# Kernel optimization log

Measured on AMD Instinct MI355X. Metric: run time of the kernel, lower is better.

Reference implementation:

```python
import jax, jax.numpy as jnp
import numpy as np

B, N, C = 4, 1029, 1024
H = 16           # num_heads
L = 8            # num_blocks
DH = C // H      # head_dim = 64
HID = 4 * C      # mlp hidden
SCALE = DH ** -0.5
EPS = 1e-6


def _ln(x, w, b):
    mu = jnp.mean(x, axis=-1, keepdims=True)
    var = jnp.var(x, axis=-1, keepdims=True)
    return (x - mu) * jax.lax.rsqrt(var + EPS) * w + b


def setup_inputs() -> dict:
    key = jax.random.key(0)
    ks = jax.random.split(key, 16)
    s = 0.02
    return {
        "x": jax.random.normal(ks[0], (B, N, C), dtype=jnp.float32),
        "ln1_w": jnp.ones((L, C), jnp.float32),
        "ln1_b": jnp.zeros((L, C), jnp.float32),
        "qkv_w": jax.random.normal(ks[1], (L, 3 * C, C), jnp.float32) * s,
        "qkv_b": jnp.zeros((L, 3 * C), jnp.float32),
        "proj_w": jax.random.normal(ks[2], (L, C, C), jnp.float32) * s,
        "proj_b": jnp.zeros((L, C), jnp.float32),
        "ln2_w": jnp.ones((L, C), jnp.float32),
        "ln2_b": jnp.zeros((L, C), jnp.float32),
        "fc1_w": jax.random.normal(ks[3], (L, HID, C), jnp.float32) * s,
        "fc1_b": jnp.zeros((L, HID), jnp.float32),
        "fc2_w": jax.random.normal(ks[4], (L, C, HID), jnp.float32) * s,
        "fc2_b": jnp.zeros((L, C), jnp.float32),
        "norm_w": jnp.ones((C,), jnp.float32),
        "norm_b": jnp.zeros((C,), jnp.float32),
    }


def _block(x, p):
    ln1_w, ln1_b, qkv_w, qkv_b, proj_w, proj_b, ln2_w, ln2_b, fc1_w, fc1_b, fc2_w, fc2_b = p
    # --- attention (manual fp32 QK^T / softmax / AV, as in Attention.forward) ---
    h = _ln(x, ln1_w, ln1_b)
    qkv = h @ qkv_w.T + qkv_b                        # [B,N,3C]
    qkv = qkv.reshape(B, N, 3, H, DH).transpose(2, 0, 3, 1, 4)  # [3,B,H,N,DH]
    q, k, v = qkv[0], qkv[1], qkv[2]
    attn = jnp.einsum("bhnd,bhmd->bhnm", q.astype(jnp.float32), k.astype(jnp.float32)) * SCALE
    # original subtracts row max before softmax; jax.nn.softmax is the same stable math
    attn = jax.nn.softmax(attn, axis=-1).astype(v.dtype)
    o = jnp.einsum("bhnm,bhmd->bhnd", attn, v)       # [B,H,N,DH]
    o = o.transpose(0, 2, 1, 3).reshape(B, N, C)
    x = x + (o @ proj_w.T + proj_b)
    # --- MLP (exact GELU, as nn.GELU default) ---
    h = _ln(x, ln2_w, ln2_b)
    h = jax.nn.gelu(h @ fc1_w.T + fc1_b, approximate=False)
    x = x + (h @ fc2_w.T + fc2_b)
    return x


def reference(x, ln1_w, ln1_b, qkv_w, qkv_b, proj_w, proj_b, ln2_w, ln2_b,
              fc1_w, fc1_b, fc2_w, fc2_b, norm_w, norm_b):
    params = (ln1_w, ln1_b, qkv_w, qkv_b, proj_w, proj_b, ln2_w, ln2_b,
              fc1_w, fc1_b, fc2_w, fc2_b)

    def body(h, p):
        return _block(h, p), None

    x, _ = jax.lax.scan(body, x, params)
    return _ln(x, norm_w, norm_b)
```

## Files before the change

kernel.cpp:

```cpp
#include <hip/hip_runtime.h>
#include <cstdint>
#include <cstddef>

#define B_    4
#define N_TOK 1029
#define C_    1024
#define H_    16
#define L_    8
#define HID_  4096
#define M_TOK (B_*N_TOK)
#define MP2_  4352
#define TM0_  4096
#define PROWS 4224
#define KVB_  128
#define KVT2_ 9
#define KPAD_ 1152

typedef float f32x4 __attribute__((ext_vector_type(4)));
typedef short bf16x8 __attribute__((ext_vector_type(8)));

__device__ __forceinline__ uint16_t f2bf(float f) {
  uint32_t u = __float_as_uint(f);
  u += 0x7fffu + ((u >> 16) & 1u);
  return (uint16_t)(u >> 16);
}

__device__ __forceinline__ void async_copy16(const uint16_t* src, uint16_t* lds_dst) {
  __builtin_amdgcn_global_load_lds(
      (const __attribute__((address_space(1))) void*)src,
      (__attribute__((address_space(3))) void*)lds_dst, 16, 0, 0);
}

__device__ __forceinline__ int swz16(int row, int byte_in_row) {
  return row * 128 + (byte_in_row ^ ((row & 7) << 4));
}

__global__ __launch_bounds__(256)
void cvt_f32_bf16(const float* __restrict__ in, uint16_t* __restrict__ out, int n4) {
  int i = blockIdx.x * 256 + threadIdx.x;
  if (i < n4) {
    float4 v = reinterpret_cast<const float4*>(in)[i];
    uint64_t pk = (uint64_t)f2bf(v.x) | ((uint64_t)f2bf(v.y) << 16)
                | ((uint64_t)f2bf(v.z) << 32) | ((uint64_t)f2bf(v.w) << 48);
    reinterpret_cast<uint64_t*>(out)[i] = pk;
  }
}

template<int OUTMODE>
__global__ __launch_bounds__(256)
void ln_fwd(const float* __restrict__ x, const float* __restrict__ w,
            const float* __restrict__ b, void* __restrict__ outp) {
  const int row = blockIdx.x;
  const int tid = threadIdx.x;
  const float4 v = reinterpret_cast<const float4*>(x + (size_t)row * C_)[tid];
  float s  = v.x + v.y + v.z + v.w;
  float s2 = v.x*v.x + v.y*v.y + v.z*v.z + v.w*v.w;
  #pragma unroll
  for (int d = 1; d < 64; d <<= 1) {
    s  += __shfl_xor(s, d);
    s2 += __shfl_xor(s2, d);
  }
  __shared__ float red[8];
  const int wv = tid >> 6;
  if ((tid & 63) == 0) { red[wv] = s; red[wv + 4] = s2; }
  __syncthreads();
  s  = red[0] + red[1] + red[2] + red[3];
  s2 = red[4] + red[5] + red[6] + red[7];
  const float mu = s * (1.0f / C_);
  const float rs = rsqrtf(fmaxf(s2 * (1.0f / C_) - mu * mu, 0.0f) + 1e-6f);
  const float4 wv4 = reinterpret_cast<const float4*>(w)[tid];
  const float4 bv4 = reinterpret_cast<const float4*>(b)[tid];
  const float o0 = (v.x - mu) * rs * wv4.x + bv4.x;
  const float o1 = (v.y - mu) * rs * wv4.y + bv4.y;
  const float o2 = (v.z - mu) * rs * wv4.z + bv4.z;
  const float o3 = (v.w - mu) * rs * wv4.w + bv4.w;
  uint64_t pk = (uint64_t)f2bf(o0) | ((uint64_t)f2bf(o1) << 16)
              | ((uint64_t)f2bf(o2) << 32) | ((uint64_t)f2bf(o3) << 48);
  reinterpret_cast<uint64_t*>((uint16_t*)outp + (size_t)row * C_)[tid] = pk;
}

template<int KCH, int OUT>
__global__ __launch_bounds__(256)
void reduce_ln(const float* __restrict__ pbuf, const float* __restrict__ bias,
               float* __restrict__ xbuf, const float* __restrict__ lw,
               const float* __restrict__ lb, void* __restrict__ outp) {
  const int m = blockIdx.x;
  const int c4 = threadIdx.x;
  float4 s = reinterpret_cast<const float4*>(bias)[c4];
  #pragma unroll
  for (int kc = 0; kc < KCH; ++kc) {
    const float4 pv = reinterpret_cast<const float4*>(pbuf + ((size_t)kc * PROWS + m) * C_)[c4];
    s.x += pv.x; s.y += pv.y; s.z += pv.z; s.w += pv.w;
  }
  float4 x = reinterpret_cast<float4*>(xbuf + (size_t)m * C_)[c4];
  x.x += s.x; x.y += s.y; x.z += s.z; x.w += s.w;
  reinterpret_cast<float4*>(xbuf + (size_t)m * C_)[c4] = x;
  float ss  = x.x + x.y + x.z + x.w;
  float ss2 = x.x*x.x + x.y*x.y + x.z*x.z + x.w*x.w;
  #pragma unroll
  for (int d = 1; d < 64; d <<= 1) {
    ss  += __shfl_xor(ss, d);
    ss2 += __shfl_xor(ss2, d);
  }
  __shared__ float red[8];
  const int wv = c4 >> 6;
  if ((c4 & 63) == 0) { red[wv] = ss; red[wv + 4] = ss2; }
  __syncthreads();
  ss  = red[0] + red[1] + red[2] + red[3];
  ss2 = red[4] + red[5] + red[6] + red[7];
  const float mu = ss * (1.0f / C_);
  const float rs = rsqrtf(fmaxf(ss2 * (1.0f / C_) - mu * mu, 0.0f) + 1e-6f);
  const float4 wv4 = reinterpret_cast<const float4*>(lw)[c4];
  const float4 bv4 = reinterpret_cast<const float4*>(lb)[c4];
  const float o0 = (x.x - mu) * rs * wv4.x + bv4.x;
  const float o1 = (x.y - mu) * rs * wv4.y + bv4.y;
  const float o2 = (x.z - mu) * rs * wv4.z + bv4.z;
  const float o3 = (x.w - mu) * rs * wv4.w + bv4.w;
  if (OUT == 0) {
    uint64_t pk = (uint64_t)f2bf(o0) | ((uint64_t)f2bf(o1) << 16)
                | ((uint64_t)f2bf(o2) << 32) | ((uint64_t)f2bf(o3) << 48);
    reinterpret_cast<uint64_t*>((uint16_t*)outp + (size_t)m * C_)[c4] = pk;
  } else {
    float4 o; o.x = o0; o.y = o1; o.z = o2; o.w = o3;
    reinterpret_cast<float4*>((float*)outp + (size_t)m * C_)[c4] = o;
  }
}

template<int EPI>
__device__ __forceinline__ void epi_store(int m, int col, float v, int Nn, int kc,
    const float* bias, uint16_t* outb, float* pbuf,
    uint16_t* Qp, uint16_t* Kp, uint16_t* VTp) {
  if (EPI == 3) {
    pbuf[((size_t)kc * PROWS + m) * C_ + col] = v;
  } else if (EPI == 1) {
    const float vb = v + bias[col];
    const float u = -1.5957691216f * (vb + 0.044715f * vb * vb * vb);
    const float g = vb * __builtin_amdgcn_rcpf(1.0f + __expf(u));
    outb[(size_t)m * Nn + col] = f2bf(g);
  } else {
    if (m < M_TOK) {
      const float vb = v + bias[col];
      const int which = col >> 10;
      const int h = (col >> 6) & 15;
      const int d = col & 63;
      const int b = m / N_TOK;
      const int key = m - b * N_TOK;
      const int bh = b * 16 + h;
      if (which == 0)      Qp[((size_t)bh * KPAD_ + key) * 64 + d] = f2bf(vb * 0.125f);
      else if (which == 1) Kp[((size_t)bh * KPAD_ + key) * 64 + d] = f2bf(vb);
      else                 VTp[((size_t)bh * 64 + d) * KPAD_ + key] = f2bf(vb);
    }
  }
}

template<int EPI, int SPLIT>
__global__ __launch_bounds__(512, 4)
void gemm_s(const uint16_t* __restrict__ A, const uint16_t* __restrict__ W,
            const float* __restrict__ bias, uint16_t* __restrict__ outb,
            float* __restrict__ pbuf, int Nn, int Ktot) {
  const int nbn = Nn >> 8;
  const int KC = Ktot / SPLIT;
  const int nwg = (int)gridDim.x;
  const int q8 = nwg >> 3, r8 = nwg & 7;
  const int xcd = (int)blockIdx.x & 7, pos = (int)blockIdx.x >> 3;
  const int wgid = (xcd < r8 ? xcd * (q8 + 1) : r8 * (q8 + 1) + (xcd - r8) * q8) + pos;
  const int kc  = wgid / (33 * nbn);
  const int rem = wgid % (33 * nbn);
  const int bm = rem % 33, bn = rem / 33;

  const int tid = (int)threadIdx.x;
  const int l = tid & 63, w = tid >> 6;
  const int l15 = l & 15, l4 = l >> 4;
  const int wr = w >> 2, wc = w & 3;

  __shared__ char lds[49152];

  const uint16_t* Ag = A + (size_t)bm * 128 * Ktot + (size_t)kc * KC;
  const uint16_t* Wg = W + (size_t)bn * 256 * Ktot + (size_t)kc * KC;

  const int srow = tid >> 3;
  const int schunk = (tid & 7) ^ (srow & 7);
  const int csel0 = ((l4) ^ (l15 & 7)) << 4;
  const int csel1 = ((4 + l4) ^ (l15 & 7)) << 4;

  f32x4 acc[4][4] = {};
  const int nt = KC >> 6;
  for (int t = 0; t < nt; ++t) {
    const int toff = t * 64;
    __syncthreads();
    #pragma unroll
    for (int j = 0; j < 2; ++j) {
      const int row = j * 64 + srow;
      async_copy16(Ag + (size_t)row * Ktot + toff + schunk * 8,
                   (uint16_t*)(lds + j * 8192 + tid * 16));
    }
    #pragma unroll
    for (int j = 0; j < 4; ++j) {
      const int row = j * 64 + srow;
      async_copy16(Wg + (size_t)row * Ktot + toff + schunk * 8,
                   (uint16_t*)(lds + 16384 + j * 8192 + tid * 16));
    }
    __syncthreads();
    #pragma unroll
    for (int kk = 0; kk < 2; ++kk) {
      const int cs = kk ? csel1 : csel0;
      bf16x8 afr[4], bfr[4];
      #pragma unroll
      for (int f = 0; f < 4; ++f)
        afr[f] = *(const bf16x8*)(lds + (wr * 64 + f * 16 + l15) * 128 + cs);
      #pragma unroll
      for (int nf = 0; nf < 4; ++nf)
        bfr[nf] = *(const bf16x8*)(lds + 16384 + (wc * 64 + nf * 16 + l15) * 128 + cs);
      #pragma unroll
      for (int f = 0; f < 4; ++f)
        #pragma unroll
        for (int nf = 0; nf < 4; ++nf)
          acc[f][nf] = __builtin_amdgcn_mfma_f32_16x16x32_bf16(afr[f], bfr[nf], acc[f][nf], 0, 0, 0);
    }
  }

  #pragma unroll
  for (int nf = 0; nf < 4; ++nf) {
    const int col = bn * 256 + wc * 64 + nf * 16 + l15;
    #pragma unroll
    for (int mf = 0; mf < 4; ++mf) {
      const int mb = bm * 128 + wr * 64 + mf * 16 + l4 * 4;
      #pragma unroll
      for (int r = 0; r < 4; ++r)
        epi_store<EPI>(mb + r, col, acc[mf][nf][r], Nn, kc, bias, outb, pbuf,
                       nullptr, nullptr, nullptr);
    }
  }
}

template<int EPI, int SPLIT>
__global__ __launch_bounds__(512)
void gemm8p(const uint16_t* __restrict__ A, const uint16_t* __restrict__ W,
            const float* __restrict__ bias, uint16_t* __restrict__ outb,
            float* __restrict__ pbuf,
            uint16_t* __restrict__ Qp, uint16_t* __restrict__ Kp,
            uint16_t* __restrict__ VTp, int Nn, int Ktot) {
  const int nbn = Nn >> 8;
  const int MAIN = 16 * nbn * SPLIT;
  const int KC = Ktot / SPLIT;
  const int nwg = (int)gridDim.x;
  const int q8 = nwg >> 3, r8 = nwg & 7;
  const int xcd = (int)blockIdx.x & 7, pos = (int)blockIdx.x >> 3;
  const int wgid = (xcd < r8 ? xcd * (q8 + 1) : r8 * (q8 + 1) + (xcd - r8) * q8) + pos;
  const int tid = (int)threadIdx.x;

  if (wgid >= MAIN) {
    if (tid >= 256) return;
    const int tailid = wgid - MAIN;
    const int tnb = Nn >> 7;
    const int tbn = tailid % tnb, tkc = tailid / tnb;
    const int l = tid & 63, w2 = tid >> 6;
    const int l15 = l & 15, l4 = l >> 4;
    const int wr = w2 >> 1, wc = w2 & 1;
    const uint16_t* Ag = A + (size_t)(TM0_ + wr * 64) * Ktot + (size_t)tkc * KC;
    const uint16_t* Wg = W + (size_t)(tbn * 128 + wc * 64) * Ktot + (size_t)tkc * KC;
    f32x4 acc[4][4] = {};
    const int ks = KC >> 5;
    for (int s = 0; s < ks; ++s) {
      bf16x8 af[4], bf[4];
      #pragma unroll
      for (int i = 0; i < 4; ++i)
        af[i] = *(const bf16x8*)(Ag + (size_t)(i * 16 + l15) * Ktot + s * 32 + l4 * 8);
      #pragma unroll
      for (int j = 0; j < 4; ++j)
        bf[j] = *(const bf16x8*)(Wg + (size_t)(j * 16 + l15) * Ktot + s * 32 + l4 * 8);
      #pragma unroll
      for (int i = 0; i < 4; ++i)
        #pragma unroll
        for (int j = 0; j < 4; ++j)
          acc[i][j] = __builtin_amdgcn_mfma_f32_16x16x32_bf16(af[i], bf[j], acc[i][j], 0, 0, 0);
    }
    #pragma unroll
    for (int j = 0; j < 4; ++j) {
      const int col = tbn * 128 + wc * 64 + j * 16 + l15;
      #pragma unroll
      for (int i = 0; i < 4; ++i)
        #pragma unroll
        for (int r = 0; r < 4; ++r) {
          const int m = TM0_ + wr * 64 + i * 16 + l4 * 4 + r;
          epi_store<EPI>(m, col, acc[i][j][r], Nn, tkc, bias, outb, pbuf, Qp, Kp, VTp);
        }
    }
    return;
  }

  __shared__ char lds[131072];
  const int kc  = (SPLIT > 1) ? wgid / (16 * nbn) : 0;
  const int rem = (SPLIT > 1) ? wgid % (16 * nbn) : wgid;
  const int bm = rem & 15, bn = rem >> 4;
  const int l = tid & 63, w = tid >> 6;
  const int l15 = l & 15, l4 = l >> 4;
  const int wr = w >> 2, wc = w & 3;

  const uint16_t* Ag = A + (size_t)bm * 256 * Ktot + (size_t)kc * KC;
  const uint16_t* Wg = W + (size_t)bn * 256 * Ktot + (size_t)kc * KC;

  const int srow = tid >> 3;
  const int schunk = (tid & 7) ^ (srow & 7);
  auto stage = [&](int mat, int j, int toff, int pdst) {
    const int rbase = mat ? (j * 64) : ((j & 1) * 128 + ((j >> 1)) * 64);
    const uint16_t* src = (mat ? Wg : Ag)
        + (size_t)(rbase + srow) * Ktot + toff + schunk * 8;
    uint16_t* dst = (uint16_t*)(lds + pdst * 65536 + mat * 32768 + rbase * 128 + tid * 16);
    async_copy16(src, dst);
  };

  const int csel0 = ((l4) ^ (l15 & 7)) * 16;
  const int csel1 = ((4 + l4) ^ (l15 & 7)) * 16;

  f32x4 acc[8][4] = {};
  stage(1, 0, 0, 0); stage(1, 1, 0, 0); stage(1, 2, 0, 0); stage(1, 3, 0, 0);
  stage(0, 0, 0, 0); stage(0, 1, 0, 0); stage(0, 2, 0, 0); stage(0, 3, 0, 0);

  const int nt = KC >> 6;
  bf16x8 bfr[2][4];
  for (int t = 0; t < nt; ++t) {
    const int p = t & 1;
    const char* base = lds + p * 65536;
    const int toff = (t + 1) * 64;
    const bool more = (t + 1 < nt);
    asm volatile("s_waitcnt vmcnt(2)" ::: "memory");
    __builtin_amdgcn_sched_barrier(0);
    __builtin_amdgcn_s_barrier();
    bf16x8 afr[4][2];
    #pragma unroll
    for (int f = 0; f < 4; ++f) {
      const int rb = (wr * 128 + f * 16 + l15) * 128;
      afr[f][0] = *(const bf16x8*)(base + rb + csel0);
      afr[f][1] = *(const bf16x8*)(base + rb + csel1);
    }
    #pragma unroll
    for (int nf = 0; nf < 4; ++nf) {
      const int rb = 32768 + (wc * 64 + nf * 16 + l15) * 128;
      bfr[0][nf] = *(const bf16x8*)(base + rb + csel0);
      bfr[1][nf] = *(const bf16x8*)(base + rb + csel1);
    }
    if (more) {
      stage(1, 0, toff, p ^ 1); stage(1, 1, toff, p ^ 1);
      stage(1, 2, toff, p ^ 1); stage(1, 3, toff, p ^ 1);
      stage(0, 0, toff, p ^ 1); stage(0, 1, toff, p ^ 1);
    }
    __builtin_amdgcn_s_setprio(1);
    #pragma unroll
    for (int kk = 0; kk < 2; ++kk)
      #pragma unroll
      for (int f = 0; f < 4; ++f)
        #pragma unroll
        for (int nf = 0; nf < 4; ++nf)
          acc[f][nf] = __builtin_amdgcn_mfma_f32_16x16x32_bf16(afr[f][kk], bfr[kk][nf], acc[f][nf], 0, 0, 0);
    __builtin_amdgcn_s_setprio(0);
    if (t == nt - 1) asm volatile("s_waitcnt vmcnt(0)" ::: "memory");
    else             asm volatile("s_waitcnt vmcnt(6)" ::: "memory");
    __builtin_amdgcn_sched_barrier(0);
    __builtin_amdgcn_s_barrier();
    #pragma unroll
    for (int f = 0; f < 4; ++f) {
      const int rb = (wr * 128 + 64 + f * 16 + l15) * 128;
      afr[f][0] = *(const bf16x8*)(base + rb + csel0);
      afr[f][1] = *(const bf16x8*)(base + rb + csel1);
    }
    if (more) { stage(0, 2, toff, p ^ 1); stage(0, 3, toff, p ^ 1); }
    __builtin_amdgcn_s_setprio(1);
    #pragma unroll
    for (int kk = 0; kk < 2; ++kk)
      #pragma unroll
      for (int f = 0; f < 4; ++f)
        #pragma unroll
        for (int nf = 0; nf < 4; ++nf)
          acc[4 + f][nf] = __builtin_amdgcn_mfma_f32_16x16x32_bf16(afr[f][kk], bfr[kk][nf], acc[4 + f][nf], 0, 0, 0);
    __builtin_amdgcn_s_setprio(0);
  }

  #pragma unroll
  for (int nf = 0; nf < 4; ++nf) {
    const int col = bn * 256 + wc * 64 + nf * 16 + l15;
    #pragma unroll
    for (int mf = 0; mf < 8; ++mf) {
      const int mb = bm * 256 + wr * 128 + mf * 16 + l4 * 4;
      #pragma unroll
      for (int r = 0; r < 4; ++r)
        epi_store<EPI>(mb + r, col, acc[mf][nf][r], Nn, kc, bias, outb, pbuf, Qp, Kp, VTp);
    }
  }
}

__global__ __launch_bounds__(256, 3)
void attn_fwd(const uint16_t* __restrict__ Qp, const uint16_t* __restrict__ Kp,
              const uint16_t* __restrict__ VTp, uint16_t* __restrict__ ob) {
  __shared__ uint16_t Ksm_[KVB_ * 64];
  __shared__ uint16_t Vsm_[64 * KVB_];
  __shared__ uint16_t Psm_[4][16 * 136];

  const int tid = (int)threadIdx.x;
  const int l = tid & 63, w = tid >> 6;
  const int l15 = l & 15, l4 = l >> 4;
  const int bh = (int)blockIdx.x;
  const int qt = (int)blockIdx.y;

  const uint16_t* Kb = Kp + (size_t)bh * KPAD_ * 64;
  const uint16_t* Vb = VTp + (size_t)bh * 64 * KPAD_;

  bf16x8 qf[2];
  {
    const int qrow = qt * 64 + w * 16 + l15;
    const uint16_t* qbase = Qp + ((size_t)bh * KPAD_ + qrow) * 64;
    qf[0] = *(const bf16x8*)(qbase + l4 * 8);
    qf[1] = *(const bf16x8*)(qbase + 32 + l4 * 8);
  }

  float mrow = -1e30f, lrow = 0.0f;
  f32x4 oacc[4] = {};

  const int krow_s = tid >> 3;
  const int kslot_s = (tid & 7) ^ (krow_s & 7);
  const int vd_s = tid >> 4;
  const int vslot_s = (tid & 15) ^ (vd_s & 15);

  for (int kt = 0; kt < KVT2_; ++kt) {
    const int key0 = kt * KVB_;
    __syncthreads();
    #pragma unroll
    for (int it = 0; it < 4; ++it) {
      const int row = it * 32 + krow_s;
      async_copy16(Kb + (size_t)(key0 + row) * 64 + kslot_s * 8,
                   Ksm_ + it * 2048 + tid * 8);
    }
    #pragma unroll
    for (int it = 0; it < 4; ++it) {
      const int d = it * 16 + vd_s;
      async_copy16(Vb + (size_t)d * KPAD_ + key0 + vslot_s * 8,
                   Vsm_ + it * 2048 + tid * 8);
    }
    __syncthreads();

    f32x4 s[8];
    #pragma unroll
    for (int kf = 0; kf < 8; ++kf) s[kf] = f32x4{0.f, 0.f, 0.f, 0.f};
    #pragma unroll
    for (int kk = 0; kk < 2; ++kk) {
      #pragma unroll
      for (int kf = 0; kf < 8; ++kf) {
        const bf16x8 kfrag = *(const bf16x8*)((const char*)Ksm_ + swz16(kf * 16 + l15, kk * 64 + l4 * 16));
        s[kf] = __builtin_amdgcn_mfma_f32_16x16x32_bf16(kfrag, qf[kk], s[kf], 0, 0, 0);
      }
    }
    if (kt == KVT2_ - 1) {
      #pragma unroll
      for (int kf = 0; kf < 8; ++kf)
        #pragma unroll
        for (int r = 0; r < 4; ++r)
          if (key0 + kf * 16 + l4 * 4 + r >= N_TOK) s[kf][r] = -1e30f;
    }
    float pmx = s[0][0];
    #pragma unroll
    for (int kf = 0; kf < 8; ++kf)
      #pragma unroll
      for (int r = 0; r < 4; ++r) pmx = fmaxf(pmx, s[kf][r]);
    pmx = fmaxf(pmx, __shfl_xor(pmx, 16));
    pmx = fmaxf(pmx, __shfl_xor(pmx, 32));
    if (!__all(pmx - mrow <= 8.0f)) {
      const float mi = fmaxf(mrow, pmx);
      const float sc = __expf(mrow - mi);
      mrow = mi;
      lrow *= sc;
      #pragma unroll
      for (int df = 0; df < 4; ++df)
        #pragma unroll
        for (int r = 0; r < 4; ++r) oacc[df][r] *= sc;
    }
    float psum = 0.0f;
    #pragma unroll
    for (int kf = 0; kf < 8; ++kf) {
      const float p0 = __expf(s[kf][0] - mrow);
      const float p1 = __expf(s[kf][1] - mrow);
      const float p2 = __expf(s[kf][2] - mrow);
      const float p3 = __expf(s[kf][3] - mrow);
      psum += (p0 + p1) + (p2 + p3);
      const uint64_t pk = (uint64_t)f2bf(p0) | ((uint64_t)f2bf(p1) << 16)
                        | ((uint64_t)f2bf(p2) << 32) | ((uint64_t)f2bf(p3) << 48);
      *(uint64_t*)(&Psm_[w][l15 * 136 + kf * 16 + l4 * 4]) = pk;
    }
    psum += __shfl_xor(psum, 16);
    psum += __shfl_xor(psum, 32);
    lrow += psum;
    #pragma unroll
    for (int kk = 0; kk < 4; ++kk) {
      const bf16x8 pf = *(const bf16x8*)(&Psm_[w][l15 * 136 + kk * 32 + l4 * 8]);
      #pragma unroll
      for (int df = 0; df < 4; ++df) {
        const int d = df * 16 + l15;
        const bf16x8 vfrag = *(const bf16x8*)(Vsm_ + d * KVB_ + (((kk * 4 + l4) ^ (d & 15)) * 8));
        oacc[df] = __builtin_amdgcn_mfma_f32_16x16x32_bf16(vfrag, pf, oacc[df], 0, 0, 0);
      }
    }
  }

  const int q = qt * 64 + w * 16 + l15;
  if (q < N_TOK) {
    const float inv = 1.0f / lrow;
    const int m = (bh >> 4) * N_TOK + q;
    const int hbase = (bh & 15) * 64;
    #pragma unroll
    for (int df = 0; df < 4; ++df)
      #pragma unroll
      for (int r = 0; r < 4; ++r) {
        const int c = hbase + df * 16 + l4 * 4 + r;
        ob[(size_t)m * C_ + c] = f2bf(oacc[df][r] * inv);
      }
  }
}

extern "C" void kernel_launch(void* const* d_in, const int* in_sizes, int n_in,
                              void* d_out, int out_size, void* d_ws, size_t ws_size,
                              hipStream_t stream) {
  const float* x_in   = (const float*)d_in[0];
  const float* ln1_w  = (const float*)d_in[1];
  const float* ln1_b  = (const float*)d_in[2];
  const float* qkv_w  = (const float*)d_in[3];
  const float* qkv_b  = (const float*)d_in[4];
  const float* proj_w = (const float*)d_in[5];
  const float* proj_b = (const float*)d_in[6];
  const float* ln2_w  = (const float*)d_in[7];
  const float* ln2_b  = (const float*)d_in[8];
  const float* fc1_w  = (const float*)d_in[9];
  const float* fc1_b  = (const float*)d_in[10];
  const float* fc2_w  = (const float*)d_in[11];
  const float* fc2_b  = (const float*)d_in[12];
  const float* norm_w = (const float*)d_in[13];
  const float* norm_b = (const float*)d_in[14];

  char* p = (char*)d_ws;
  float*    xbuf = (float*)p;     p += (size_t)MP2_ * C_ * 4;
  uint16_t* hbuf = (uint16_t*)p;  p += (size_t)MP2_ * C_ * 2;
  uint16_t* big  = (uint16_t*)p;  p += (size_t)MP2_ * HID_ * 2;
  uint16_t* wq   = (uint16_t*)p;  p += (size_t)L_ * 3 * C_ * C_ * 2;
  uint16_t* wp   = (uint16_t*)p;  p += (size_t)L_ * C_ * C_ * 2;
  uint16_t* w1   = (uint16_t*)p;  p += (size_t)L_ * HID_ * C_ * 2;
  uint16_t* w2   = (uint16_t*)p;  p += (size_t)L_ * C_ * HID_ * 2;
  uint16_t* qp   = (uint16_t*)p;  p += (size_t)64 * KPAD_ * 64 * 2;
  uint16_t* kp   = (uint16_t*)p;  p += (size_t)64 * KPAD_ * 64 * 2;
  uint16_t* vtp  = (uint16_t*)p;  p += (size_t)64 * 64 * KPAD_ * 2;
  float*    pbuf = (float*)p;     p += (size_t)4 * PROWS * C_ * 4;
  if ((size_t)(p - (char*)d_ws) > ws_size) return;

  hipMemcpyAsync(xbuf, x_in, (size_t)M_TOK * C_ * sizeof(float),
                 hipMemcpyDeviceToDevice, stream);

  auto cvt = [&](const float* src, uint16_t* dst, size_t n) {
    const int n4 = (int)(n / 4);
    cvt_f32_bf16<<<dim3((n4 + 255) / 256), dim3(256), 0, stream>>>(src, dst, n4);
  };
  cvt(qkv_w,  wq, (size_t)L_ * 3 * C_ * C_);
  cvt(proj_w, wp, (size_t)L_ * C_ * C_);
  cvt(fc1_w,  w1, (size_t)L_ * HID_ * C_);
  cvt(fc2_w,  w2, (size_t)L_ * C_ * HID_);

  ln_fwd<0><<<dim3(M_TOK), dim3(256), 0, stream>>>(xbuf, ln1_w, ln1_b, hbuf);

  for (int lyr = 0; lyr < L_; ++lyr) {
    gemm8p<0, 1><<<dim3(216), dim3(512), 0, stream>>>(
        hbuf, wq + (size_t)lyr * 3 * C_ * C_, qkv_b + (size_t)lyr * 3 * C_,
        nullptr, nullptr, qp, kp, vtp, 3 * C_, C_);
    attn_fwd<<<dim3(64, 17), dim3(256), 0, stream>>>(qp, kp, vtp, hbuf);
    gemm_s<3, 4><<<dim3(528), dim3(512), 0, stream>>>(
        hbuf, wp + (size_t)lyr * C_ * C_, nullptr, nullptr, pbuf, C_, C_);
    reduce_ln<4, 0><<<dim3(M_TOK), dim3(256), 0, stream>>>(
        pbuf, proj_b + (size_t)lyr * C_, xbuf,
        ln2_w + (size_t)lyr * C_, ln2_b + (size_t)lyr * C_, hbuf);
    gemm_s<1, 1><<<dim3(528), dim3(512), 0, stream>>>(
        hbuf, w1 + (size_t)lyr * HID_ * C_, fc1_b + (size_t)lyr * HID_,
        big, nullptr, HID_, C_);
    gemm_s<3, 4><<<dim3(528), dim3(512), 0, stream>>>(
        big, w2 + (size_t)lyr * C_ * HID_, nullptr, nullptr, pbuf, C_, HID_);
    if (lyr < L_ - 1) {
      reduce_ln<4, 0><<<dim3(M_TOK), dim3(256), 0, stream>>>(
          pbuf, fc2_b + (size_t)lyr * C_, xbuf,
          ln1_w + (size_t)(lyr + 1) * C_, ln1_b + (size_t)(lyr + 1) * C_, hbuf);
    } else {
      reduce_ln<4, 1><<<dim3(M_TOK), dim3(256), 0, stream>>>(
          pbuf, fc2_b + (size_t)lyr * C_, xbuf, norm_w, norm_b, d_out);
    }
  }
}
```

Measured before the change: 2.675 ms.

## Register-prefetch gemm_s mainloop, drop gemm8p, retune QKV/proj splits

Replaces the synchronous global_load_lds staging in gemm_s with a register prefetch: the next K tile is loaded into registers while MFMAs run on the current LDS tile, then written to LDS after the barrier. Removes the specialized 256x256 double-buffered gemm8p kernel and its tail path, routing the QKV projection through gemm_s with a 128x256 tiling (396 workgroups). Changes the proj GEMM split-K from 4 to 2 with a matching reduce. Trades more VGPR pressure and explicit LDS stores for latency hiding, and loses the larger tile reuse gemm8p had for QKV.

```diff
diff --git a/kernel.cpp b/kernel.cpp
--- a/kernel.cpp
+++ b/kernel.cpp
@@ -10,7 +10,6 @@
 #define HID_  4096
 #define M_TOK (B_*N_TOK)
 #define MP2_  4352
-#define TM0_  4096
 #define PROWS 4224
 #define KVB_  128
 #define KVT2_ 9
@@ -157,7 +156,9 @@
 __global__ __launch_bounds__(512, 4)
 void gemm_s(const uint16_t* __restrict__ A, const uint16_t* __restrict__ W,
             const float* __restrict__ bias, uint16_t* __restrict__ outb,
-            float* __restrict__ pbuf, int Nn, int Ktot) {
+            float* __restrict__ pbuf, int Nn, int Ktot,
+            uint16_t* __restrict__ Qp, uint16_t* __restrict__ Kp,
+            uint16_t* __restrict__ VTp) {
   const int nbn = Nn >> 8;
   const int KC = Ktot / SPLIT;
   const int nwg = (int)gridDim.x;
@@ -183,24 +184,30 @@
   const int csel0 = ((l4) ^ (l15 & 7)) << 4;
   const int csel1 = ((4 + l4) ^ (l15 & 7)) << 4;
 
+  bf16x8 rA0, rA1, rB0, rB1, rB2, rB3;
+  auto gload = [&](int toff) {
+    rA0 = *(const bf16x8*)(Ag + (size_t)(srow)      * Ktot + toff + schunk * 8);
+    rA1 = *(const bf16x8*)(Ag + (size_t)(64 + srow) * Ktot + toff + schunk * 8);
+    rB0 = *(const bf16x8*)(Wg + (size_t)(srow)       * Ktot + toff + schunk * 8);
+    rB1 = *(const bf16x8*)(Wg + (size_t)(64 + srow)  * Ktot + toff + schunk * 8);
+    rB2 = *(const bf16x8*)(Wg + (size_t)(128 + srow) * Ktot + toff + schunk * 8);
+    rB3 = *(const bf16x8*)(Wg + (size_t)(192 + srow) * Ktot + toff + schunk * 8);
+  };
+
   f32x4 acc[4][4] = {};
   const int nt = KC >> 6;
+  gload(0);
   for (int t = 0; t < nt; ++t) {
-    const int toff = t * 64;
     __syncthreads();
-    #pragma unroll
-    for (int j = 0; j < 2; ++j) {
-      const int row = j * 64 + srow;
-      async_copy16(Ag + (size_t)row * Ktot + toff + schunk * 8,
-                   (uint16_t*)(lds + j * 8192 + tid * 16));
-    }
-    #pragma unroll
-    for (int j = 0; j < 4; ++j) {
-      const int row = j * 64 + srow;
-      async_copy16(Wg + (size_t)row * Ktot + toff + schunk * 8,
-                   (uint16_t*)(lds + 16384 + j * 8192 + tid * 16));
-    }
+    *(bf16x8*)(lds +         tid * 16) = rA0;
+    *(bf16x8*)(lds +  8192 + tid * 16) = rA1;
+    *(bf16x8*)(lds + 16384 + tid * 16) = rB0;
+    *(bf16x8*)(lds + 24576 + tid * 16) = rB1;
+    *(bf16x8*)(lds + 32768 + tid * 16) = rB2;
+    *(bf16x8*)(lds + 40960 + tid * 16) = rB3;
     __syncthreads();
+    if (t + 1 < nt) gload((t + 1) * 64);
+    __builtin_amdgcn_sched_barrier(0);
     #pragma unroll
     for (int kk = 0; kk < 2; ++kk) {
       const int cs = kk ? csel1 : csel0;
@@ -228,163 +235,7 @@
       #pragma unroll
       for (int r = 0; r < 4; ++r)
         epi_store<EPI>(mb + r, col, acc[mf][nf][r], Nn, kc, bias, outb, pbuf,
-                       nullptr, nullptr, nullptr);
-    }
-  }
-}
-
-template<int EPI, int SPLIT>
-__global__ __launch_bounds__(512)
-void gemm8p(const uint16_t* __restrict__ A, const uint16_t* __restrict__ W,
-            const float* __restrict__ bias, uint16_t* __restrict__ outb,
-            float* __restrict__ pbuf,
-            uint16_t* __restrict__ Qp, uint16_t* __restrict__ Kp,
-            uint16_t* __restrict__ VTp, int Nn, int Ktot) {
-  const int nbn = Nn >> 8;
-  const int MAIN = 16 * nbn * SPLIT;
-  const int KC = Ktot / SPLIT;
-  const int nwg = (int)gridDim.x;
-  const int q8 = nwg >> 3, r8 = nwg & 7;
-  const int xcd = (int)blockIdx.x & 7, pos = (int)blockIdx.x >> 3;
-  const int wgid = (xcd < r8 ? xcd * (q8 + 1) : r8 * (q8 + 1) + (xcd - r8) * q8) + pos;
-  const int tid = (int)threadIdx.x;
-
-  if (wgid >= MAIN) {
-    if (tid >= 256) return;
-    const int tailid = wgid - MAIN;
-    const int tnb = Nn >> 7;
-    const int tbn = tailid % tnb, tkc = tailid / tnb;
-    const int l = tid & 63, w2 = tid >> 6;
-    const int l15 = l & 15, l4 = l >> 4;
-    const int wr = w2 >> 1, wc = w2 & 1;
-    const uint16_t* Ag = A + (size_t)(TM0_ + wr * 64) * Ktot + (size_t)tkc * KC;
-    const uint16_t* Wg = W + (size_t)(tbn * 128 + wc * 64) * Ktot + (size_t)tkc * KC;
-    f32x4 acc[4][4] = {};
-    const int ks = KC >> 5;
-    for (int s = 0; s < ks; ++s) {
-      bf16x8 af[4], bf[4];
-      #pragma unroll
-      for (int i = 0; i < 4; ++i)
-        af[i] = *(const bf16x8*)(Ag + (size_t)(i * 16 + l15) * Ktot + s * 32 + l4 * 8);
-      #pragma unroll
-      for (int j = 0; j < 4; ++j)
-        bf[j] = *(const bf16x8*)(Wg + (size_t)(j * 16 + l15) * Ktot + s * 32 + l4 * 8);
-      #pragma unroll
-      for (int i = 0; i < 4; ++i)
-        #pragma unroll
-        for (int j = 0; j < 4; ++j)
-          acc[i][j] = __builtin_amdgcn_mfma_f32_16x16x32_bf16(af[i], bf[j], acc[i][j], 0, 0, 0);
-    }
-    #pragma unroll
-    for (int j = 0; j < 4; ++j) {
-      const int col = tbn * 128 + wc * 64 + j * 16 + l15;
-      #pragma unroll
-      for (int i = 0; i < 4; ++i)
-        #pragma unroll
-        for (int r = 0; r < 4; ++r) {
-          const int m = TM0_ + wr * 64 + i * 16 + l4 * 4 + r;
-          epi_store<EPI>(m, col, acc[i][j][r], Nn, tkc, bias, outb, pbuf, Qp, Kp, VTp);
-        }
-    }
-    return;
-  }
-
-  __shared__ char lds[131072];
-  const int kc  = (SPLIT > 1) ? wgid / (16 * nbn) : 0;
-  const int rem = (SPLIT > 1) ? wgid % (16 * nbn) : wgid;
-  const int bm = rem & 15, bn = rem >> 4;
-  const int l = tid & 63, w = tid >> 6;
-  const int l15 = l & 15, l4 = l >> 4;
-  const int wr = w >> 2, wc = w & 3;
-
-  const uint16_t* Ag = A + (size_t)bm * 256 * Ktot + (size_t)kc * KC;
-  const uint16_t* Wg = W + (size_t)bn * 256 * Ktot + (size_t)kc * KC;
-
-  const int srow = tid >> 3;
-  const int schunk = (tid & 7) ^ (srow & 7);
-  auto stage = [&](int mat, int j, int toff, int pdst) {
-    const int rbase = mat ? (j * 64) : ((j & 1) * 128 + ((j >> 1)) * 64);
-    const uint16_t* src = (mat ? Wg : Ag)
-        + (size_t)(rbase + srow) * Ktot + toff + schunk * 8;
-    uint16_t* dst = (uint16_t*)(lds + pdst * 65536 + mat * 32768 + rbase * 128 + tid * 16);
-    async_copy16(src, dst);
-  };
-
-  const int csel0 = ((l4) ^ (l15 & 7)) * 16;
-  const int csel1 = ((4 + l4) ^ (l15 & 7)) * 16;
-
-  f32x4 acc[8][4] = {};
-  stage(1, 0, 0, 0); stage(1, 1, 0, 0); stage(1, 2, 0, 0); stage(1, 3, 0, 0);
-  stage(0, 0, 0, 0); stage(0, 1, 0, 0); stage(0, 2, 0, 0); stage(0, 3, 0, 0);
-
-  const int nt = KC >> 6;
-  bf16x8 bfr[2][4];
-  for (int t = 0; t < nt; ++t) {
-    const int p = t & 1;
-    const char* base = lds + p * 65536;
-    const int toff = (t + 1) * 64;
-    const bool more = (t + 1 < nt);
-    asm volatile("s_waitcnt vmcnt(2)" ::: "memory");
-    __builtin_amdgcn_sched_barrier(0);
-    __builtin_amdgcn_s_barrier();
-    bf16x8 afr[4][2];
-    #pragma unroll
-    for (int f = 0; f < 4; ++f) {
-      const int rb = (wr * 128 + f * 16 + l15) * 128;
-      afr[f][0] = *(const bf16x8*)(base + rb + csel0);
-      afr[f][1] = *(const bf16x8*)(base + rb + csel1);
-    }
-    #pragma unroll
-    for (int nf = 0; nf < 4; ++nf) {
-      const int rb = 32768 + (wc * 64 + nf * 16 + l15) * 128;
-      bfr[0][nf] = *(const bf16x8*)(base + rb + csel0);
-      bfr[1][nf] = *(const bf16x8*)(base + rb + csel1);
-    }
-    if (more) {
-      stage(1, 0, toff, p ^ 1); stage(1, 1, toff, p ^ 1);
-      stage(1, 2, toff, p ^ 1); stage(1, 3, toff, p ^ 1);
-      stage(0, 0, toff, p ^ 1); stage(0, 1, toff, p ^ 1);
-    }
-    __builtin_amdgcn_s_setprio(1);
-    #pragma unroll
-    for (int kk = 0; kk < 2; ++kk)
-      #pragma unroll
-      for (int f = 0; f < 4; ++f)
-        #pragma unroll
-        for (int nf = 0; nf < 4; ++nf)
-          acc[f][nf] = __builtin_amdgcn_mfma_f32_16x16x32_bf16(afr[f][kk], bfr[kk][nf], acc[f][nf], 0, 0, 0);
-    __builtin_amdgcn_s_setprio(0);
-    if (t == nt - 1) asm volatile("s_waitcnt vmcnt(0)" ::: "memory");
-    else             asm volatile("s_waitcnt vmcnt(6)" ::: "memory");
-    __builtin_amdgcn_sched_barrier(0);
-    __builtin_amdgcn_s_barrier();
-    #pragma unroll
-    for (int f = 0; f < 4; ++f) {
-      const int rb = (wr * 128 + 64 + f * 16 + l15) * 128;
-      afr[f][0] = *(const bf16x8*)(base + rb + csel0);
-      afr[f][1] = *(const bf16x8*)(base + rb + csel1);
-    }
-    if (more) { stage(0, 2, toff, p ^ 1); stage(0, 3, toff, p ^ 1); }
-    __builtin_amdgcn_s_setprio(1);
-    #pragma unroll
-    for (int kk = 0; kk < 2; ++kk)
-      #pragma unroll
-      for (int f = 0; f < 4; ++f)
-        #pragma unroll
-        for (int nf = 0; nf < 4; ++nf)
-          acc[4 + f][nf] = __builtin_amdgcn_mfma_f32_16x16x32_bf16(afr[f][kk], bfr[kk][nf], acc[4 + f][nf], 0, 0, 0);
-    __builtin_amdgcn_s_setprio(0);
-  }
-
-  #pragma unroll
-  for (int nf = 0; nf < 4; ++nf) {
-    const int col = bn * 256 + wc * 64 + nf * 16 + l15;
-    #pragma unroll
-    for (int mf = 0; mf < 8; ++mf) {
-      const int mb = bm * 256 + wr * 128 + mf * 16 + l4 * 4;
-      #pragma unroll
-      for (int r = 0; r < 4; ++r)
-        epi_store<EPI>(mb + r, col, acc[mf][nf][r], Nn, kc, bias, outb, pbuf, Qp, Kp, VTp);
+                       Qp, Kp, VTp);
     }
   }
 }
@@ -563,20 +414,22 @@
   ln_fwd<0><<<dim3(M_TOK), dim3(256), 0, stream>>>(xbuf, ln1_w, ln1_b, hbuf);
 
   for (int lyr = 0; lyr < L_; ++lyr) {
-    gemm8p<0, 1><<<dim3(216), dim3(512), 0, stream>>>(
+    gemm_s<0, 1><<<dim3(396), dim3(512), 0, stream>>>(
         hbuf, wq + (size_t)lyr * 3 * C_ * C_, qkv_b + (size_t)lyr * 3 * C_,
-        nullptr, nullptr, qp, kp, vtp, 3 * C_, C_);
+        nullptr, nullptr, 3 * C_, C_, qp, kp, vtp);
     attn_fwd<<<dim3(64, 17), dim3(256), 0, stream>>>(qp, kp, vtp, hbuf);
-    gemm_s<3, 4><<<dim3(528), dim3(512), 0, stream>>>(
-        hbuf, wp + (size_t)lyr * C_ * C_, nullptr, nullptr, pbuf, C_, C_);
-    reduce_ln<4, 0><<<dim3(M_TOK), dim3(256), 0, stream>>>(
+    gemm_s<3, 2><<<dim3(264), dim3(512), 0, stream>>>(
+        hbuf, wp + (size_t)lyr * C_ * C_, nullptr, nullptr, pbuf, C_, C_,
+        nullptr, nullptr, nullptr);
+    reduce_ln<2, 0><<<dim3(M_TOK), dim3(256), 0, stream>>>(
         pbuf, proj_b + (size_t)lyr * C_, xbuf,
         ln2_w + (size_t)lyr * C_, ln2_b + (size_t)lyr * C_, hbuf);
     gemm_s<1, 1><<<dim3(528), dim3(512), 0, stream>>>(
         hbuf, w1 + (size_t)lyr * HID_ * C_, fc1_b + (size_t)lyr * HID_,
-        big, nullptr, HID_, C_);
+        big, nullptr, HID_, C_, nullptr, nullptr, nullptr);
     gemm_s<3, 4><<<dim3(528), dim3(512), 0, stream>>>(
-        big, w2 + (size_t)lyr * C_ * HID_, nullptr, nullptr, pbuf, C_, HID_);
+        big, w2 + (size_t)lyr * C_ * HID_, nullptr, nullptr, pbuf, C_, HID_,
+        nullptr, nullptr, nullptr);
     if (lyr < L_ - 1) {
       reduce_ln<4, 0><<<dim3(M_TOK), dim3(256), 0, stream>>>(
           pbuf, fc2_b + (size_t)lyr * C_, xbuf,
```

Measured after the change: 2.473 ms, median of 2. 7.5% less time.
